# Optimization experiments

Measured on AMD Instinct MI355X. Metric: run time of the kernel, lower is better.

The kernel has to match this reference:

```python
import jax, jax.numpy as jnp
import numpy as np

B, T, D, H = 2048, 2048, 3, 32  # batch, time steps, input_size, hidden_size


def setup_inputs() -> dict:
    key = jax.random.key(0)
    k0, k1, k2, k3, k4 = jax.random.split(key, 5)
    lim = 1.0 / np.sqrt(H)  # eqx.nn.GRUCell init range
    inp = jax.random.normal(k0, (B, T, D), dtype=jnp.float32)
    weight_ih = jax.random.uniform(k1, (3 * H, D), minval=-lim, maxval=lim, dtype=jnp.float32)
    weight_hh = jax.random.uniform(k2, (3 * H, H), minval=-lim, maxval=lim, dtype=jnp.float32)
    bias = jax.random.uniform(k3, (3 * H,), minval=-lim, maxval=lim, dtype=jnp.float32)
    bias_n = jax.random.uniform(k4, (H,), minval=-lim, maxval=lim, dtype=jnp.float32)
    return {"inp": inp, "weight_ih": weight_ih, "weight_hh": weight_hh,
            "bias": bias, "bias_n": bias_n}


def reference(inp, weight_ih, weight_hh, bias, bias_n):
    # inp: [B, T, D]. Faithful batched version of PinnWithGRU.__call__:
    # scan an eqx.nn.GRUCell over time from a zero hidden state, output hidden[0] per step.
    b = inp.shape[0]
    h0 = jnp.zeros((b, H), dtype=inp.dtype)
    xs = jnp.swapaxes(inp, 0, 1)  # [T, B, D]

    def step(h, x):
        ig = x @ weight_ih.T + bias      # [B, 3H] input gates (+ bias, as in eqx)
        hg = h @ weight_hh.T             # [B, 3H] hidden gates
        ir, iz, ia = jnp.split(ig, 3, axis=-1)
        hr, hz, ha = jnp.split(hg, 3, axis=-1)
        r = jax.nn.sigmoid(ir + hr)
        z = jax.nn.sigmoid(iz + hz)
        n = jnp.tanh(ia + bias_n + r * ha)
        h_new = (1.0 - z) * n + z * h
        return h_new, h_new[:, 0]        # emit first hidden unit per step

    _, out = jax.lax.scan(step, h0, xs)  # out: [T, B]
    return jnp.swapaxes(out, 0, 1)[..., None]  # [B, T, 1] (matches per-seq [T, 1])
```

## Files before the change

kernel.cpp:

```cpp
#include <hip/hip_runtime.h>


#define GRU_B 2048
#define GRU_T 2048
#define GRU_D 3
#define GRU_H 32
#define CHUNK 32

#define WAIT_LGKM0 0xC07F

__device__ __forceinline__ float fast_sigmoid(float x) {
    float e = __expf(-x);
    return __builtin_amdgcn_rcpf(1.0f + e);
}
__device__ __forceinline__ float fast_tanh(float x) {
    float e = __expf(2.0f * x);
    return 1.0f - 2.0f * __builtin_amdgcn_rcpf(e + 1.0f);
}
__device__ __forceinline__ float xor32(float v, int paddr) {
    return __int_as_float(__builtin_amdgcn_ds_bpermute(paddr, __float_as_int(v)));
}

__global__ __launch_bounds__(64, 2) void gru_scan_kernel(
    const float* __restrict__ inp,
    const float* __restrict__ w_ih,
    const float* __restrict__ w_hh,
    const float* __restrict__ bias,
    const float* __restrict__ bias_n,
    float* __restrict__ out)
{
    __shared__ __align__(16) float h2[4 * GRU_H];
    __shared__ __align__(16) float x_lds[CHUNK * GRU_D];

    const int lane  = threadIdx.x;
    const int unit  = lane & 31;
    const int half  = lane >> 5;
    const int b     = blockIdx.x;
    const int paddr = (lane ^ 32) << 2;

    const int rowA = unit + 32 * half;
    const int rowB = unit + 32 * (1 - half);
    const int rowC = 2 * GRU_H + unit;
    const int kofs = 16 * half;

    float wa[16], wb[16], wc[16];
    {
        const float4* pa = (const float4*)(w_hh + (size_t)rowA * GRU_H + kofs);
        const float4* pb = (const float4*)(w_hh + (size_t)rowB * GRU_H + kofs);
        const float4* pc = (const float4*)(w_hh + (size_t)rowC * GRU_H + kofs);
#pragma unroll
        for (int q = 0; q < 4; ++q) {
            float4 A = pa[q], Bv = pb[q], Cv = pc[q];
            wa[4*q+0]=A.x;  wa[4*q+1]=A.y;  wa[4*q+2]=A.z;  wa[4*q+3]=A.w;
            wb[4*q+0]=Bv.x; wb[4*q+1]=Bv.y; wb[4*q+2]=Bv.z; wb[4*q+3]=Bv.w;
            wc[4*q+0]=Cv.x; wc[4*q+1]=Cv.y; wc[4*q+2]=Cv.z; wc[4*q+3]=Cv.w;
        }
    }
    float wia[GRU_D], wic[GRU_D];
#pragma unroll
    for (int d = 0; d < GRU_D; ++d) {
        wia[d] = w_ih[(size_t)rowA * GRU_D + d];
        wic[d] = w_ih[(size_t)rowC * GRU_D + d];
    }
    const float bA = bias[rowA];
    const float bC = bias[rowC] + bias_n[unit];

    const float* xb = inp + (size_t)b * GRU_T * GRU_D;
    float*       ob = out + (size_t)b * GRU_T;

    float h = 0.0f;
    float outreg = 0.0f;

    h2[lane] = 0.0f;
    __builtin_amdgcn_s_waitcnt(WAIT_LGKM0);

    const float4* hv = (const float4*)(h2 + 48 * half);
    const int wbase = unit + 64 * half;

    for (int c = 0; c < GRU_T / CHUNK; ++c) {
        {
            const int base = c * (CHUNK * GRU_D);
            x_lds[lane] = xb[base + lane];
            if (lane < CHUNK * GRU_D - 64) x_lds[64 + lane] = xb[base + 64 + lane];
        }
        __builtin_amdgcn_s_waitcnt(WAIT_LGKM0);

#pragma unroll 8
        for (int s = 0; s < CHUNK; ++s) {
            float hk[16];
#pragma unroll
            for (int q = 0; q < 4; ++q) {
                float4 v = hv[q];
                hk[4*q+0]=v.x; hk[4*q+1]=v.y; hk[4*q+2]=v.z; hk[4*q+3]=v.w;
            }
            const float x0 = x_lds[3 * s + 0];
            const float x1 = x_lds[3 * s + 1];
            const float x2 = x_lds[3 * s + 2];

            const float aM = fmaf(wia[2], x2, fmaf(wia[1], x1, fmaf(wia[0], x0, bA)));
            const float aN = fmaf(wic[2], x2, fmaf(wic[1], x1, fmaf(wic[0], x0, bC)));

            float A = 0.0f, Bp = 0.0f, Cp = 0.0f;
#pragma unroll
            for (int k = 0; k < 16; ++k) {
                A  = fmaf(wa[k], hk[k], A);
                Bp = fmaf(wb[k], hk[k], Bp);
                Cp = fmaf(wc[k], hk[k], Cp);
            }
            const float gM = A  + xor32(Bp, paddr);
            const float gN = Cp + xor32(Cp, paddr);

            const float sg  = fast_sigmoid(aM + gM);
            const float zsw = xor32(sg, paddr);
            const float n   = fast_tanh(fmaf(sg, gN, aN));
            const float hnew = fmaf(zsw, h - n, n);

            if (lane == s - 1) outreg = hk[0];

            h = hnew;
            h2[wbase]      = h;
            h2[wbase + 32] = h;
            __builtin_amdgcn_s_waitcnt(WAIT_LGKM0);
        }

        {
            const float h0 = h2[0];
            if (lane == CHUNK - 1) outreg = h0;
        }
        if (lane < CHUNK) ob[c * CHUNK + lane] = outreg;
    }
}

extern "C" void kernel_launch(void* const* d_in, const int* in_sizes, int n_in,
                              void* d_out, int out_size, void* d_ws, size_t ws_size,
                              hipStream_t stream) {
    const float* inp    = (const float*)d_in[0];
    const float* w_ih   = (const float*)d_in[1];
    const float* w_hh   = (const float*)d_in[2];
    const float* bias   = (const float*)d_in[3];
    const float* bias_n = (const float*)d_in[4];
    float* out = (float*)d_out;

    dim3 grid(GRU_B);
    dim3 block(64);
    gru_scan_kernel<<<grid, block, 0, stream>>>(inp, w_ih, w_hh, bias, bias_n, out);
}
```

Baseline: 708.6 us.

## Compute full r/z dot per lane, split accumulators, prefetch inputs

Each lane now holds a full 32-wide row of the r or z gate weights and computes its whole dot product locally. This removes the cross-half bpermute reduction that used to sit on the serial recurrence path; only the candidate gate still uses a half-split reduction. The dot products use four independent accumulators to shorten the FMA dependency chain. The next chunk's inputs are prefetched into registers, and the duplicated LDS hidden-state write and the explicit waitcnts are dropped. In exchange each lane holds more weight registers and reads more hidden state from LDS per step, which may raise register pressure.

```diff
diff --git a/kernel.cpp b/kernel.cpp
--- a/kernel.cpp
+++ b/kernel.cpp
@@ -29,7 +29,7 @@
     const float* __restrict__ bias_n,
     float* __restrict__ out)
 {
-    __shared__ __align__(16) float h2[4 * GRU_H];
+    __shared__ __align__(16) float h2[2 * GRU_H];
     __shared__ __align__(16) float x_lds[CHUNK * GRU_D];
 
     const int lane  = threadIdx.x;
@@ -38,32 +38,33 @@
     const int b     = blockIdx.x;
     const int paddr = (lane ^ 32) << 2;
 
-    const int rowA = unit + 32 * half;
-    const int rowB = unit + 32 * (1 - half);
-    const int rowC = 2 * GRU_H + unit;
+    const int rowS = unit + 32 * half;
+    const int rowN = 2 * GRU_H + unit;
     const int kofs = 16 * half;
 
-    float wa[16], wb[16], wc[16];
+    float ws[32], wn[16];
     {
-        const float4* pa = (const float4*)(w_hh + (size_t)rowA * GRU_H + kofs);
-        const float4* pb = (const float4*)(w_hh + (size_t)rowB * GRU_H + kofs);
-        const float4* pc = (const float4*)(w_hh + (size_t)rowC * GRU_H + kofs);
+        const float4* ps = (const float4*)(w_hh + (size_t)rowS * GRU_H);
+#pragma unroll
+        for (int q = 0; q < 8; ++q) {
+            float4 v = ps[q];
+            ws[4*q+0]=v.x; ws[4*q+1]=v.y; ws[4*q+2]=v.z; ws[4*q+3]=v.w;
+        }
+        const float4* pn = (const float4*)(w_hh + (size_t)rowN * GRU_H + kofs);
 #pragma unroll
         for (int q = 0; q < 4; ++q) {
-            float4 A = pa[q], Bv = pb[q], Cv = pc[q];
-            wa[4*q+0]=A.x;  wa[4*q+1]=A.y;  wa[4*q+2]=A.z;  wa[4*q+3]=A.w;
-            wb[4*q+0]=Bv.x; wb[4*q+1]=Bv.y; wb[4*q+2]=Bv.z; wb[4*q+3]=Bv.w;
-            wc[4*q+0]=Cv.x; wc[4*q+1]=Cv.y; wc[4*q+2]=Cv.z; wc[4*q+3]=Cv.w;
+            float4 v = pn[q];
+            wn[4*q+0]=v.x; wn[4*q+1]=v.y; wn[4*q+2]=v.z; wn[4*q+3]=v.w;
         }
     }
-    float wia[GRU_D], wic[GRU_D];
+    float wis[GRU_D], win[GRU_D];
 #pragma unroll
     for (int d = 0; d < GRU_D; ++d) {
-        wia[d] = w_ih[(size_t)rowA * GRU_D + d];
-        wic[d] = w_ih[(size_t)rowC * GRU_D + d];
+        wis[d] = w_ih[(size_t)rowS * GRU_D + d];
+        win[d] = w_ih[(size_t)rowN * GRU_D + d];
     }
-    const float bA = bias[rowA];
-    const float bC = bias[rowC] + bias_n[unit];
+    const float bS = bias[rowS];
+    const float bN = bias[rowN] + bias_n[unit];
 
     const float* xb = inp + (size_t)b * GRU_T * GRU_D;
     float*       ob = out + (size_t)b * GRU_T;
@@ -74,53 +75,73 @@
     h2[lane] = 0.0f;
     __builtin_amdgcn_s_waitcnt(WAIT_LGKM0);
 
-    const float4* hv = (const float4*)(h2 + 48 * half);
-    const int wbase = unit + 64 * half;
+    const float4* hv  = (const float4*)h2;
+    const float4* hvn = (const float4*)(h2 + kofs);
+    const int wbase = unit + 32 * half;
+
+    float xr0 = xb[lane];
+    float xr1 = (lane < CHUNK * GRU_D - 64) ? xb[64 + lane] : 0.0f;
 
     for (int c = 0; c < GRU_T / CHUNK; ++c) {
-        {
-            const int base = c * (CHUNK * GRU_D);
-            x_lds[lane] = xb[base + lane];
-            if (lane < CHUNK * GRU_D - 64) x_lds[64 + lane] = xb[base + 64 + lane];
+        x_lds[lane] = xr0;
+        if (lane < CHUNK * GRU_D - 64) x_lds[64 + lane] = xr1;
+        if (c + 1 < GRU_T / CHUNK) {
+            const int nb = (c + 1) * (CHUNK * GRU_D);
+            xr0 = xb[nb + lane];
+            xr1 = (lane < CHUNK * GRU_D - 64) ? xb[nb + 64 + lane] : 0.0f;
         }
-        __builtin_amdgcn_s_waitcnt(WAIT_LGKM0);
 
 #pragma unroll 8
         for (int s = 0; s < CHUNK; ++s) {
-            float hk[16];
+            float hk[32];
 #pragma unroll
-            for (int q = 0; q < 4; ++q) {
+            for (int q = 0; q < 8; ++q) {
                 float4 v = hv[q];
                 hk[4*q+0]=v.x; hk[4*q+1]=v.y; hk[4*q+2]=v.z; hk[4*q+3]=v.w;
             }
-            const float x0 = x_lds[3 * s + 0];
-            const float x1 = x_lds[3 * s + 1];
-            const float x2 = x_lds[3 * s + 2];
+            float hn[16];
+#pragma unroll
+            for (int q = 0; q < 4; ++q) {
+                float4 v = hvn[q];
+                hn[4*q+0]=v.x; hn[4*q+1]=v.y; hn[4*q+2]=v.z; hn[4*q+3]=v.w;
+            }
+            const float x0 = x_lds[3*s+0];
+            const float x1 = x_lds[3*s+1];
+            const float x2 = x_lds[3*s+2];
 
-            const float aM = fmaf(wia[2], x2, fmaf(wia[1], x1, fmaf(wia[0], x0, bA)));
-            const float aN = fmaf(wic[2], x2, fmaf(wic[1], x1, fmaf(wic[0], x0, bC)));
+            const float aS = fmaf(wis[2], x2, fmaf(wis[1], x1, fmaf(wis[0], x0, bS)));
+            const float aN = fmaf(win[2], x2, fmaf(win[1], x1, fmaf(win[0], x0, bN)));
 
-            float A = 0.0f, Bp = 0.0f, Cp = 0.0f;
+            float N0=0.0f, N1=0.0f, N2=0.0f, N3=0.0f;
 #pragma unroll
-            for (int k = 0; k < 16; ++k) {
-                A  = fmaf(wa[k], hk[k], A);
-                Bp = fmaf(wb[k], hk[k], Bp);
-                Cp = fmaf(wc[k], hk[k], Cp);
+            for (int q = 0; q < 4; ++q) {
+                N0 = fmaf(wn[4*q+0], hn[4*q+0], N0);
+                N1 = fmaf(wn[4*q+1], hn[4*q+1], N1);
+                N2 = fmaf(wn[4*q+2], hn[4*q+2], N2);
+                N3 = fmaf(wn[4*q+3], hn[4*q+3], N3);
             }
-            const float gM = A  + xor32(Bp, paddr);
-            const float gN = Cp + xor32(Cp, paddr);
+            const float Np = (N0 + N1) + (N2 + N3);
+            const float gN = Np + xor32(Np, paddr);
 
-            const float sg  = fast_sigmoid(aM + gM);
-            const float zsw = xor32(sg, paddr);
-            const float n   = fast_tanh(fmaf(sg, gN, aN));
-            const float hnew = fmaf(zsw, h - n, n);
+            float S0=aS, S1=0.0f, S2=0.0f, S3=0.0f;
+#pragma unroll
+            for (int q = 0; q < 8; ++q) {
+                S0 = fmaf(ws[4*q+0], hk[4*q+0], S0);
+                S1 = fmaf(ws[4*q+1], hk[4*q+1], S1);
+                S2 = fmaf(ws[4*q+2], hk[4*q+2], S2);
+                S3 = fmaf(ws[4*q+3], hk[4*q+3], S3);
+            }
+            const float S = (S0 + S1) + (S2 + S3);
+
+            const float sg = fast_sigmoid(S);
+            const float zc = xor32(sg, paddr);
+            const float n  = fast_tanh(fmaf(sg, gN, aN));
+            const float hnew = fmaf(zc, h - n, n);
 
             if (lane == s - 1) outreg = hk[0];
 
             h = hnew;
-            h2[wbase]      = h;
-            h2[wbase + 32] = h;
-            __builtin_amdgcn_s_waitcnt(WAIT_LGKM0);
+            h2[wbase] = h;
         }
 
         {
```

New measurement: 1.012 ms. +42.9%, slower.

## Use permlane32_swap for half-wave exchange, prefetch inputs, simplify h layout

Applied to the files above, without the earlier changes.

Replaces the ds_bpermute lane-xor-32 exchanges with the gfx950 permlane32_swap instruction, which stays on the VALU path instead of going through LDS. A runtime probe picks which output half of the swap to use, falling back to bpermute if neither matches. The hidden-state buffer shrinks to a single 64-entry copy, each step's explicit LDS waitcnt is dropped, and the next chunk's inputs are prefetched into registers. The dot products are split into two accumulators to shorten FMA dependency chains. Dropping the per-step waitcnt relies on the compiler inserting waits itself for the LDS read-after-write, and the three template instantiations increase code size.

```diff
diff --git a/kernel.cpp b/kernel.cpp
--- a/kernel.cpp
+++ b/kernel.cpp
@@ -9,6 +9,8 @@
 
 #define WAIT_LGKM0 0xC07F
 
+typedef unsigned int uint2v __attribute__((ext_vector_type(2)));
+
 __device__ __forceinline__ float fast_sigmoid(float x) {
     float e = __expf(-x);
     return __builtin_amdgcn_rcpf(1.0f + e);
@@ -17,8 +19,95 @@
     float e = __expf(2.0f * x);
     return 1.0f - 2.0f * __builtin_amdgcn_rcpf(e + 1.0f);
 }
-__device__ __forceinline__ float xor32(float v, int paddr) {
-    return __int_as_float(__builtin_amdgcn_ds_bpermute(paddr, __float_as_int(v)));
+
+template<int MODE>
+__device__ __forceinline__ float xswap(float v, int lane, int paddr) {
+    if constexpr (MODE == 2) {
+        return __int_as_float(__builtin_amdgcn_ds_bpermute(paddr, __float_as_int(v)));
+    } else {
+        uint2v r = __builtin_amdgcn_permlane32_swap(
+            __float_as_uint(v), __float_as_uint(v), false, false);
+        const unsigned lo = (MODE == 0) ? r.x : r.y;
+        const unsigned hi = (MODE == 0) ? r.y : r.x;
+        return __uint_as_float((lane < 32) ? lo : hi);
+    }
+}
+
+template<int MODE>
+__device__ __forceinline__ void gru_loop(
+    const float* __restrict__ xb, float* __restrict__ ob,
+    float* __restrict__ h2, float* __restrict__ x_lds,
+    const float* __restrict__ wa, const float* __restrict__ wb,
+    const float* __restrict__ wc,
+    const float* __restrict__ wia, const float* __restrict__ wic,
+    float bA, float bC, int lane, int half, int paddr)
+{
+    const float4* hv = (const float4*)(h2 + 16 * half);
+
+    float h = 0.0f;
+    float outreg = 0.0f;
+
+    float xr0 = xb[lane];
+    float xr1 = (lane < CHUNK * GRU_D - 64) ? xb[64 + lane] : 0.0f;
+
+    for (int c = 0; c < GRU_T / CHUNK; ++c) {
+        x_lds[lane] = xr0;
+        if (lane < CHUNK * GRU_D - 64) x_lds[64 + lane] = xr1;
+        if (c + 1 < GRU_T / CHUNK) {
+            const int nb = (c + 1) * (CHUNK * GRU_D);
+            xr0 = xb[nb + lane];
+            xr1 = (lane < CHUNK * GRU_D - 64) ? xb[nb + 64 + lane] : 0.0f;
+        }
+
+#pragma unroll 8
+        for (int s = 0; s < CHUNK; ++s) {
+            float hk[16];
+#pragma unroll
+            for (int q = 0; q < 4; ++q) {
+                float4 v = hv[q];
+                hk[4*q+0]=v.x; hk[4*q+1]=v.y; hk[4*q+2]=v.z; hk[4*q+3]=v.w;
+            }
+            const float x0 = x_lds[3*s+0];
+            const float x1 = x_lds[3*s+1];
+            const float x2 = x_lds[3*s+2];
+
+            const float aM = fmaf(wia[2], x2, fmaf(wia[1], x1, fmaf(wia[0], x0, bA)));
+            const float aN = fmaf(wic[2], x2, fmaf(wic[1], x1, fmaf(wic[0], x0, bC)));
+
+            float A0=0.f, A1=0.f, B0=0.f, B1=0.f, C0=0.f, C1=0.f;
+#pragma unroll
+            for (int k = 0; k < 16; k += 2) {
+                A0 = fmaf(wa[k],   hk[k],   A0);
+                A1 = fmaf(wa[k+1], hk[k+1], A1);
+                B0 = fmaf(wb[k],   hk[k],   B0);
+                B1 = fmaf(wb[k+1], hk[k+1], B1);
+                C0 = fmaf(wc[k],   hk[k],   C0);
+                C1 = fmaf(wc[k+1], hk[k+1], C1);
+            }
+            const float A  = A0 + A1;
+            const float Bp = B0 + B1;
+            const float Cp = C0 + C1;
+
+            const float gM = A  + xswap<MODE>(Bp, lane, paddr);
+            const float gN = Cp + xswap<MODE>(Cp, lane, paddr);
+
+            const float sg  = fast_sigmoid(aM + gM);
+            const float zsw = xswap<MODE>(sg, lane, paddr);
+            const float n   = fast_tanh(fmaf(sg, gN, aN));
+            const float hnew = fmaf(zsw, h - n, n);
+
+            if (lane == s - 1) outreg = hk[0];
+
+            h = hnew;
+            h2[lane] = h;
+        }
+
+        {
+            const float h0 = h2[0];
+            if (lane == CHUNK - 1) outreg = h0;
+        }
+        if (lane < CHUNK) ob[c * CHUNK + lane] = outreg;
+    }
 }
 
 __global__ __launch_bounds__(64, 2) void gru_scan_kernel(
@@ -29,7 +118,7 @@
     const float* __restrict__ bias_n,
     float* __restrict__ out)
 {
-    __shared__ __align__(16) float h2[4 * GRU_H];
+    __shared__ __align__(16) float h2[2 * GRU_H];
     __shared__ __align__(16) float x_lds[CHUNK * GRU_D];
 
     const int lane  = threadIdx.x;
@@ -50,8 +139,8 @@
         const float4* pc = (const float4*)(w_hh + (size_t)rowC * GRU_H + kofs);
 #pragma unroll
         for (int q = 0; q < 4; ++q) {
-            float4 A = pa[q], Bv = pb[q], Cv = pc[q];
-            wa[4*q+0]=A.x;  wa[4*q+1]=A.y;  wa[4*q+2]=A.z;  wa[4*q+3]=A.w;
+            float4 Av = pa[q], Bv = pb[q], Cv = pc[q];
+            wa[4*q+0]=Av.x; wa[4*q+1]=Av.y; wa[4*q+2]=Av.z; wa[4*q+3]=Av.w;
             wb[4*q+0]=Bv.x; wb[4*q+1]=Bv.y; wb[4*q+2]=Bv.z; wb[4*q+3]=Bv.w;
             wc[4*q+0]=Cv.x; wc[4*q+1]=Cv.y; wc[4*q+2]=Cv.z; wc[4*q+3]=Cv.w;
         }
@@ -68,67 +157,27 @@
     const float* xb = inp + (size_t)b * GRU_T * GRU_D;
     float*       ob = out + (size_t)b * GRU_T;
 
-    float h = 0.0f;
-    float outreg = 0.0f;
-
     h2[lane] = 0.0f;
     __builtin_amdgcn_s_waitcnt(WAIT_LGKM0);
 
-    const float4* hv = (const float4*)(h2 + 48 * half);
-    const int wbase = unit + 64 * half;
+    int mode;
+    {
+        const unsigned pl = (unsigned)lane;
+        uint2v pr = __builtin_amdgcn_permlane32_swap(pl, pl, false, false);
+        const unsigned want = (unsigned)(lane ^ 32);
+        const unsigned selA = (lane < 32) ? pr.x : pr.y;
+        const unsigned selB = (lane < 32) ? pr.y : pr.x;
+        if (__ballot(selA == want) == 0xFFFFFFFFFFFFFFFFULL)      mode = 0;
+        else if (__ballot(selB == want) == 0xFFFFFFFFFFFFFFFFULL) mode = 1;
+        else                                                      mode = 2;
+    }
 
-    for (int c = 0; c < GRU_T / CHUNK; ++c) {
-        {
-            const int base = c * (CHUNK * GRU_D);
-            x_lds[lane] = xb[base + lane];
-            if (lane < CHUNK * GRU_D - 64) x_lds[64 + lane] = xb[base + 64 + lane];
-        }
-        __builtin_amdgcn_s_waitcnt(WAIT_LGKM0);
-
-#pragma unroll 8
-        for (int s = 0; s < CHUNK; ++s) {
-            float hk[16];
-#pragma unroll
-            for (int q = 0; q < 4; ++q) {
-                float4 v = hv[q];
-                hk[4*q+0]=v.x; hk[4*q+1]=v.y; hk[4*q+2]=v.z; hk[4*q+3]=v.w;
-            }
-            const float x0 = x_lds[3 * s + 0];
-            const float x1 = x_lds[3 * s + 1];
-            const float x2 = x_lds[3 * s + 2];
-
-            const float aM = fmaf(wia[2], x2, fmaf(wia[1], x1, fmaf(wia[0], x0, bA)));
-            const float aN = fmaf(wic[2], x2, fmaf(wic[1], x1, fmaf(wic[0], x0, bC)));
-
-            float A = 0.0f, Bp = 0.0f, Cp = 0.0f;
-#pragma unroll
-            for (int k = 0; k < 16; ++k) {
-                A  = fmaf(wa[k], hk[k], A);
-                Bp = fmaf(wb[k], hk[k], Bp);
-                Cp = fmaf(wc[k], hk[k], Cp);
-            }
-            const float gM = A  + xor32(Bp, paddr);
-            const float gN = Cp + xor32(Cp, paddr);
-
-            const float sg  = fast_sigmoid(aM + gM);
-            const float zsw = xor32(sg, paddr);
-            const float n   = fast_tanh(fmaf(sg, gN, aN));
-            const float hnew = fmaf(zsw, h - n, n);
-
-            if (lane == s - 1) outreg = hk[0];
-
-            h = hnew;
-            h2[wbase]      = h;
-            h2[wbase + 32] = h;
-            __builtin_amdgcn_s_waitcnt(WAIT_LGKM0);
-        }
-
-        {
-            const float h0 = h2[0];
-            if (lane == CHUNK - 1) outreg = h0;
-        }
-        if (lane < CHUNK) ob[c * CHUNK + lane] = outreg;
-    }
+    if (mode == 0)
+        gru_loop<0>(xb, ob, h2, x_lds, wa, wb, wc, wia, wic, bA, bC, lane, half, paddr);
+    else if (mode == 1)
+        gru_loop<1>(xb, ob, h2, x_lds, wa, wb, wc, wia, wic, bA, bC, lane, half, paddr);
+    else
+        gru_loop<2>(xb, ob, h2, x_lds, wa, wb, wc, wia, wic, bA, bC, lane, half, paddr);
 }
 
 extern "C" void kernel_launch(void* const* d_in, const int* in_sizes, int n_in,
```

Measured after the change: 686.1 us. 1.03x faster.

## Replace LDS hidden-state exchange with DPP row rotates and permlane swaps

Applied to the files above, without the earlier changes.

Restructures the per-step hidden-state broadcast so it no longer goes through LDS. Each 16-lane row rotates h with DPP row_ror and exchanges partial sums with permlane16/32 swaps, which removes the LDS store/wait/load round trip on the serial recurrence path. Inputs are now held in registers and read with readlane, prefetched one chunk ahead, and the chunk size doubles. A runtime probe falls back to a ds_bpermute path if the gfx950 permlane builtins behave unexpectedly, which adds code complexity and a branch-selected template instantiation.

```diff
diff --git a/kernel.cpp b/kernel.cpp
--- a/kernel.cpp
+++ b/kernel.cpp
@@ -5,9 +5,17 @@
 #define GRU_T 2048
 #define GRU_D 3
 #define GRU_H 32
-#define CHUNK 32
-
-#define WAIT_LGKM0 0xC07F
+#define CHUNK 64
+
+#if __has_builtin(__builtin_amdgcn_permlane16_swap) && \
+    __has_builtin(__builtin_amdgcn_permlane32_swap) && \
+    __has_builtin(__builtin_amdgcn_update_dpp)
+#define HAVE_FAST 1
+#else
+#define HAVE_FAST 0
+#endif
+
+typedef unsigned int uint2v __attribute__((ext_vector_type(2)));
 
 __device__ __forceinline__ float fast_sigmoid(float x) {
     float e = __expf(-x);
@@ -17,8 +25,124 @@
     float e = __expf(2.0f * x);
     return 1.0f - 2.0f * __builtin_amdgcn_rcpf(e + 1.0f);
 }
-__device__ __forceinline__ float xor32(float v, int paddr) {
-    return __int_as_float(__builtin_amdgcn_ds_bpermute(paddr, __float_as_int(v)));
+__device__ __forceinline__ float bperm(float v, int baddr) {
+    return __int_as_float(__builtin_amdgcn_ds_bpermute(baddr, __float_as_int(v)));
+}
+
+#if HAVE_FAST
+#define DPPF(v, CTRL) __int_as_float(__builtin_amdgcn_update_dpp( \
+    0, __float_as_int(v), (CTRL), 0xF, 0xF, false))
+#endif
+
+template<bool FAST>
+__device__ __forceinline__ float xsw16(float v, bool sel, int a16) {
+#if HAVE_FAST
+    if constexpr (FAST) {
+        uint2v r = __builtin_amdgcn_permlane16_swap(
+            __float_as_uint(v), __float_as_uint(v), false, false);
+        return __uint_as_float(sel ? r.x : r.y);
+    }
+#endif
+    return bperm(v, a16);
+}
+template<bool FAST>
+__device__ __forceinline__ float xsw32(float v, bool sel, int a32) {
+#if HAVE_FAST
+    if constexpr (FAST) {
+        uint2v r = __builtin_amdgcn_permlane32_swap(
+            __float_as_uint(v), __float_as_uint(v), false, false);
+        return __uint_as_float(sel ? r.x : r.y);
+    }
+#endif
+    return bperm(v, a32);
+}
+
+template<bool FAST>
+__device__ __forceinline__ void gru_loop(
+    const float* __restrict__ xb, float* __restrict__ ob,
+    const float* wsA, const float* wsB, const float* wsC,
+    const float* wiA, const float* wiC, float bA, float bC,
+    int lane, bool g, bool sel16, bool sel32, bool m12,
+    int a16, int a32, int p)
+{
+    int ra[16];
+    if constexpr (!FAST) {
+#pragma unroll
+        for (int j = 0; j < 16; ++j)
+            ra[j] = ((lane & 48) | ((p + j) & 15)) << 2;
+    }
+
+    float h = 0.0f;
+    float3 xc = *(const float3*)(xb + (size_t)lane * 3);
+
+    for (int c = 0; c < GRU_T / CHUNK; ++c) {
+        float3 xn = xc;
+        if (c + 1 < GRU_T / CHUNK)
+            xn = *(const float3*)(xb + ((size_t)(c + 1) * CHUNK + lane) * 3);
+        float outreg = 0.0f;
+
+#pragma unroll 8
+        for (int s = 0; s < CHUNK; ++s) {
+            const float x0 = __int_as_float(__builtin_amdgcn_readlane(__float_as_int(xc.x), s));
+            const float x1 = __int_as_float(__builtin_amdgcn_readlane(__float_as_int(xc.y), s));
+            const float x2 = __int_as_float(__builtin_amdgcn_readlane(__float_as_int(xc.z), s));
+
+            float hr[16];
+            hr[0] = h;
+            if constexpr (FAST) {
+#if HAVE_FAST
+                hr[1]  = DPPF(h, 0x121); hr[2]  = DPPF(h, 0x122);
+                hr[3]  = DPPF(h, 0x123); hr[4]  = DPPF(h, 0x124);
+                hr[5]  = DPPF(h, 0x125); hr[6]  = DPPF(h, 0x126);
+                hr[7]  = DPPF(h, 0x127); hr[8]  = DPPF(h, 0x128);
+                hr[9]  = DPPF(h, 0x129); hr[10] = DPPF(h, 0x12A);
+                hr[11] = DPPF(h, 0x12B); hr[12] = DPPF(h, 0x12C);
+                hr[13] = DPPF(h, 0x12D); hr[14] = DPPF(h, 0x12E);
+                hr[15] = DPPF(h, 0x12F);
+#endif
+            } else {
+#pragma unroll
+                for (int j = 1; j < 16; ++j) hr[j] = bperm(h, ra[j]);
+            }
+
+            const float aM = fmaf(wiA[2], x2, fmaf(wiA[1], x1, fmaf(wiA[0], x0, bA)));
+            const float aN = fmaf(wiC[2], x2, fmaf(wiC[1], x1, fmaf(wiC[0], x0, bC)));
+
+            float A0 = aM, A1 = 0.f, B0 = 0.f, B1 = 0.f, C0 = 0.f, C1 = 0.f;
+#pragma unroll
+            for (int j = 0; j < 16; j += 2) {
+                A0 = fmaf(wsA[j],   hr[j],   A0);
+                A1 = fmaf(wsA[j+1], hr[j+1], A1);
+                B0 = fmaf(wsB[j],   hr[j],   B0);
+                B1 = fmaf(wsB[j+1], hr[j+1], B1);
+                C0 = fmaf(wsC[j],   hr[j],   C0);
+                C1 = fmaf(wsC[j+1], hr[j+1], C1);
+            }
+            const float Bp = B0 + B1;
+            const float Cp = C0 + C1;
+            const float gM = (A0 + A1) + xsw16<FAST>(Bp, sel16, a16);
+            const float gN = Cp + xsw16<FAST>(Cp, sel16, a16);
+
+            const float hx = xsw16<FAST>(h, sel16, a16);
+            const float hprev = m12 ? hx : h;
+
+            const float sg  = fast_sigmoid(gM);
+            const float zsw = xsw16<FAST>(sg, sel16, a16);
+            const float rr = g ? zsw : sg;
+            const float zz = g ? sg : zsw;
+            const float n  = fast_tanh(fmaf(rr, gN, aN));
+            const float hnw = fmaf(zz, hprev - n, n);
+
+            const float h0 = __uint_as_float(
+                __builtin_amdgcn_readfirstlane(__float_as_uint(hnw)));
+            outreg = (lane == s) ? h0 : outreg;
+
+            const float hsw = xsw32<FAST>(hnw, sel32, a32);
+            h = m12 ? hsw : hnw;
+        }
+        ob[c * CHUNK + lane] = outreg;
+        xc = xn;
+    }
 }
 
 __global__ __launch_bounds__(64, 2) void gru_scan_kernel(
@@ -29,106 +153,74 @@
     const float* __restrict__ bias_n,
     float* __restrict__ out)
 {
-    __shared__ __align__(16) float h2[4 * GRU_H];
-    __shared__ __align__(16) float x_lds[CHUNK * GRU_D];
-
-    const int lane  = threadIdx.x;
-    const int unit  = lane & 31;
-    const int half  = lane >> 5;
-    const int b     = blockIdx.x;
-    const int paddr = (lane ^ 32) << 2;
-
-    const int rowA = unit + 32 * half;
-    const int rowB = unit + 32 * (1 - half);
-    const int rowC = 2 * GRU_H + unit;
-    const int kofs = 16 * half;
-
-    float wa[16], wb[16], wc[16];
+    const int lane = threadIdx.x;
+    const int p = lane & 15;
+    const int r = lane >> 4;
+    const int gi = r & 1;
+    const bool g = gi != 0;
+    const int o = p + 16 * (r >> 1);
+    const bool m12 = (r == 1) || (r == 2);
+    const int b = blockIdx.x;
+    const int a16 = (lane ^ 16) << 2;
+    const int a32 = (lane ^ 32) << 2;
+
+    bool fast = false, sel16 = false, sel32 = false;
+    int dir = 1;
+#if HAVE_FAST
     {
-        const float4* pa = (const float4*)(w_hh + (size_t)rowA * GRU_H + kofs);
-        const float4* pb = (const float4*)(w_hh + (size_t)rowB * GRU_H + kofs);
-        const float4* pc = (const float4*)(w_hh + (size_t)rowC * GRU_H + kofs);
-#pragma unroll
-        for (int q = 0; q < 4; ++q) {
-            float4 A = pa[q], Bv = pb[q], Cv = pc[q];
-            wa[4*q+0]=A.x;  wa[4*q+1]=A.y;  wa[4*q+2]=A.z;  wa[4*q+3]=A.w;
-            wb[4*q+0]=Bv.x; wb[4*q+1]=Bv.y; wb[4*q+2]=Bv.z; wb[4*q+3]=Bv.w;
-            wc[4*q+0]=Cv.x; wc[4*q+1]=Cv.y; wc[4*q+2]=Cv.z; wc[4*q+3]=Cv.w;
-        }
-    }
-    float wia[GRU_D], wic[GRU_D];
+        const unsigned ul = (unsigned)lane;
+        uint2v q16 = __builtin_amdgcn_permlane16_swap(ul, ul, false, false);
+        const unsigned w16 = ul ^ 16u;
+        sel16 = (q16.x == w16);
+        const bool ok16 = __ballot((q16.x == w16) || (q16.y == w16)) == ~0ULL;
+
+        uint2v q32 = __builtin_amdgcn_permlane32_swap(ul, ul, false, false);
+        const unsigned w32 = ul ^ 32u;
+        sel32 = (q32.x == w32);
+        const bool ok32 = __ballot((q32.x == w32) || (q32.y == w32)) == ~0ULL;
+
+        const int d1 = __builtin_amdgcn_update_dpp(0, p, 0x121, 0xF, 0xF, false);
+        bool okd = false;
+        if (__ballot(d1 == ((p + 1) & 15)) == ~0ULL)       { okd = true; dir = 1; }
+        else if (__ballot(d1 == ((p + 15) & 15)) == ~0ULL) { okd = true; dir = -1; }
+
+        fast = ok16 && ok32 && okd;
+    }
+#endif
+
+    const int rowA = 32 * gi + o;
+    const int rowB = 32 * (1 - gi) + o;
+    const int rowC = 2 * GRU_H + o;
+    const int kb = 16 * gi;
+    float wsA[16], wsB[16], wsC[16];
+#pragma unroll
+    for (int j = 0; j < 16; ++j) {
+        const int kk = kb + ((p + dir * j + 16) & 15);
+        wsA[j] = w_hh[rowA * GRU_H + kk];
+        wsB[j] = w_hh[rowB * GRU_H + kk];
+        wsC[j] = w_hh[rowC * GRU_H + kk];
+    }
+    float wiA[GRU_D], wiC[GRU_D];
 #pragma unroll
     for (int d = 0; d < GRU_D; ++d) {
-        wia[d] = w_ih[(size_t)rowA * GRU_D + d];
-        wic[d] = w_ih[(size_t)rowC * GRU_D + d];
+        wiA[d] = w_ih[rowA * GRU_D + d];
+        wiC[d] = w_ih[rowC * GRU_D + d];
     }
     const float bA = bias[rowA];
-    const float bC = bias[rowC] + bias_n[unit];
+    const float bC = bias[rowC] + bias_n[o];
 
     const float* xb = inp + (size_t)b * GRU_T * GRU_D;
     float*       ob = out + (size_t)b * GRU_T;
 
-    float h = 0.0f;
-    float outreg = 0.0f;
-
-    h2[lane] = 0.0f;
-    __builtin_amdgcn_s_waitcnt(WAIT_LGKM0);
-
-    const float4* hv = (const float4*)(h2 + 48 * half);
-    const int wbase = unit + 64 * half;
-
-    for (int c = 0; c < GRU_T / CHUNK; ++c) {
-        {
-            const int base = c * (CHUNK * GRU_D);
-            x_lds[lane] = xb[base + lane];
-            if (lane < CHUNK * GRU_D - 64) x_lds[64 + lane] = xb[base + 64 + lane];
-        }
-        __builtin_amdgcn_s_waitcnt(WAIT_LGKM0);
-
-#pragma unroll 8
-        for (int s = 0; s < CHUNK; ++s) {
-            float hk[16];
-#pragma unroll
-            for (int q = 0; q < 4; ++q) {
-                float4 v = hv[q];
-                hk[4*q+0]=v.x; hk[4*q+1]=v.y; hk[4*q+2]=v.z; hk[4*q+3]=v.w;
-            }
-            const float x0 = x_lds[3 * s + 0];
-            const float x1 = x_lds[3 * s + 1];
-            const float x2 = x_lds[3 * s + 2];
-
-            const float aM = fmaf(wia[2], x2, fmaf(wia[1], x1, fmaf(wia[0], x0, bA)));
-            const float aN = fmaf(wic[2], x2, fmaf(wic[1], x1, fmaf(wic[0], x0, bC)));
-
-            float A = 0.0f, Bp = 0.0f, Cp = 0.0f;
-#pragma unroll
-            for (int k = 0; k < 16; ++k) {
-                A  = fmaf(wa[k], hk[k], A);
-                Bp = fmaf(wb[k], hk[k], Bp);
-                Cp = fmaf(wc[k], hk[k], Cp);
-            }
-            const float gM = A  + xor32(Bp, paddr);
-            const float gN = Cp + xor32(Cp, paddr);
-
-            const float sg  = fast_sigmoid(aM + gM);
-            const float zsw = xor32(sg, paddr);
-            const float n   = fast_tanh(fmaf(sg, gN, aN));
-            const float hnew = fmaf(zsw, h - n, n);
-
-            if (lane == s - 1) outreg = hk[0];
-
-            h = hnew;
-            h2[wbase]      = h;
-            h2[wbase + 32] = h;
-            __builtin_amdgcn_s_waitcnt(WAIT_LGKM0);
-        }
-
-        {
-            const float h0 = h2[0];
-            if (lane == CHUNK - 1) outreg = h0;
-        }
-        if (lane < CHUNK) ob[c * CHUNK + lane] = outreg;
-    }
+#if HAVE_FAST
+    if (fast) {
+        gru_loop<true>(xb, ob, wsA, wsB, wsC, wiA, wiC, bA, bC,
+                       lane, g, sel16, sel32, m12, a16, a32, p);
+        return;
+    }
+#endif
+    gru_loop<false>(xb, ob, wsA, wsB, wsC, wiA, wiC, bA, bC,
+                    lane, g, sel16, sel32, m12, a16, a32, p);
 }
 
 extern "C" void kernel_launch(void* const* d_in, const int* in_sizes, int n_in,
```

Measured after the change: 976.9 us. +37.9%, slower.
